# Kernel optimization log

Measured on AMD Instinct MI355X. Metric: run time of the kernel, lower is better.

The kernel has to match this reference:

```python
import jax, jax.numpy as jnp
import numpy as np
import math

B, T, M, C = 4, 2048, 16, 256   # batch, seq, m chunks, c_s chunk width
DIM = 1024                       # layer width; k = DIM // C = 4
D = 64                           # conditioning bottleneck
N_ITERS, TAU = 20, 1.0


def _diag_bias(rows, cols):
    b = np.full((rows, cols), -8.0, dtype=np.float32)
    for i in range(min(rows, cols)):
        b[i, i] = 0.0
    return jnp.asarray(b)


def setup_inputs() -> dict:
    key = jax.random.key(0)
    ks = jax.random.split(key, 10)
    state_dim = M * C
    k = DIM // C
    H_post = np.full((M, k), -8.0, dtype=np.float32)
    for i in range(M):
        H_post[i, i % k] = 0.0
    return {
        "s": jax.random.normal(ks[0], (B, T, M, C), jnp.float32),
        "gamma": 0.02 * jax.random.normal(ks[1], (state_dim,), jnp.float32),
        "compress": 0.02 * jax.random.normal(ks[2], (state_dim, D), jnp.float32),
        "alpha_pre": jnp.float32(0.01),
        "to_logits_pre": 0.02 * jax.random.normal(ks[3], (D, k * M), jnp.float32),
        "H_pre": _diag_bias(k, M),
        "alpha_align": jnp.float32(0.01),
        "to_logits_align": 0.02 * jax.random.normal(ks[4], (D, M * M), jnp.float32),
        "H_align": _diag_bias(M, M),
        "alpha_next": jnp.float32(0.01),
        "to_logits_next": 0.02 * jax.random.normal(ks[5], (D, M * M), jnp.float32),
        "H_next": _diag_bias(M, M),
        "alpha_post": jnp.float32(0.01),
        "to_logits_post": 0.02 * jax.random.normal(ks[6], (D, M * k), jnp.float32),
        "H_post": jnp.asarray(H_post),
        "W_layer": jax.random.normal(ks[7], (DIM, DIM), jnp.float32) / math.sqrt(DIM),
    }


def sinkhorn_log(logits, num_iters=N_ITERS, tau=TAU):
    """Log-domain Sinkhorn; output row-scaled so row sums = 1 * rows-normalized."""
    rows, cols = logits.shape[-2], logits.shape[-1]
    Z = logits / tau
    lr = -math.log(rows)
    lc = -math.log(cols)
    u0 = jnp.zeros(Z.shape[:-1], Z.dtype)
    v0 = jnp.zeros(Z.shape[:-2] + (cols,), Z.dtype)

    def body(_, uv):
        u, v = uv
        u = lr - jax.nn.logsumexp(Z + v[..., None, :], axis=-1)
        v = lc - jax.nn.logsumexp(Z + u[..., None], axis=-2)
        return (u, v)

    u, v = jax.lax.fori_loop(0, num_iters, body, (u0, v0))
    return jnp.exp(Z + u[..., None] + v[..., None, :]) * rows


def _route(code, alpha, to_logits, bias, state, rows, cols):
    """Fused: Sinkhorn(alpha*(code@to_logits)+bias) @ state."""
    raw = (code @ to_logits).reshape(code.shape[:-1] + (rows, cols))
    P = sinkhorn_log(alpha * raw + bias)
    return jnp.einsum('...ij,...jc->...ic', P, state)


def reference(s, gamma, compress, alpha_pre, to_logits_pre, H_pre,
              alpha_align, to_logits_align, H_align,
              alpha_next, to_logits_next, H_next,
              alpha_post, to_logits_post, H_post, W_layer):
    b, t, m, c = s.shape
    state_dim = m * c
    k = W_layer.shape[0] // c
    # RMSNorm over flattened state: F.normalize * sqrt(dim) * (gamma + 1)
    s_vec = s.reshape(b, t, state_dim)
    l2 = jnp.sqrt(jnp.sum(s_vec * s_vec, axis=-1, keepdims=True))
    s_norm = s_vec / jnp.maximum(l2, 1e-12) * jnp.sqrt(jnp.float32(state_dim)) * (gamma + 1.0)
    code = s_norm @ compress  # (b, t, d)
    # read: H_pre (k x m) routes state -> layer input
    layer_in = _route(code, alpha_pre, to_logits_pre, H_pre, s, k, m).reshape(b, t, k * c)
    layer_out = layer_in @ W_layer  # the wrapped layer_fn (dense linear)
    # write: align, absorb output via H_post, prepare next via H_next
    s_aligned = _route(code, alpha_align, to_logits_align, H_align, s, m, m)
    out_flat = layer_out.reshape(b, t, k, c)
    s_updated = s_aligned + _route(code, alpha_post, to_logits_post, H_post, out_flat, m, k)
    s_next = _route(code, alpha_next, to_logits_next, H_next, s_updated, m, m)
    return s_next
```

## Files before the change

kernel.cpp:

```cpp
#include <hip/hip_runtime.h>
#include <math.h>

#define NTOK 8192
#define SD   4096
#define ITERS 20

typedef __attribute__((ext_vector_type(8))) short short8;
typedef __attribute__((ext_vector_type(8))) unsigned short ushort8;
typedef __attribute__((ext_vector_type(4))) unsigned short us4;
typedef __attribute__((ext_vector_type(4))) float f32x4;

__device__ inline unsigned short f2bf(float x) {
    unsigned int u = __float_as_uint(x);
    unsigned int r = (u + 0x7FFFu + ((u >> 16) & 1u)) >> 16;
    return (unsigned short)r;
}
__device__ inline float bf2f(unsigned short u) {
    return __uint_as_float((unsigned int)u << 16);
}

__global__ __launch_bounds__(256) void k_preall(const float* __restrict__ W, unsigned short* __restrict__ WT,
                                                const float* __restrict__ compress, const float* __restrict__ gamma,
                                                unsigned short* __restrict__ cgT,
                                                const float* __restrict__ tl_pre, const float* __restrict__ tl_al,
                                                const float* __restrict__ tl_nx,  const float* __restrict__ tl_po,
                                                unsigned short* __restrict__ tlT)
{
    const int b = blockIdx.x;
    const int tid = threadIdx.x;
    if (b < 256) {
        __shared__ float tb[64][65];
        const int k0 = (b >> 4) * 64, n0 = (b & 15) * 64;
        #pragma unroll 4
        for (int q = 0; q < 16; ++q) {
            const int idx = q * 256 + tid;
            const int r = idx >> 6, c = idx & 63;
            tb[r][c] = W[(size_t)(k0 + r) * 1024 + n0 + c];
        }
        __syncthreads();
        #pragma unroll 4
        for (int q = 0; q < 16; ++q) {
            const int idx = q * 256 + tid;
            const int n = idx >> 6, k = idx & 63;
            WT[(size_t)(n0 + n) * 1024 + k0 + k] = f2bf(tb[k][n]);
        }
    } else if (b < 320) {
        __shared__ float tb2[64][65];
        __shared__ float gsh[64];
        const int k0 = (b - 256) * 64;
        #pragma unroll 4
        for (int q = 0; q < 16; ++q) {
            const int idx = q * 256 + tid;
            const int r = idx >> 6, dd = idx & 63;
            tb2[r][dd] = compress[(size_t)(k0 + r) * 64 + dd];
        }
        if (tid < 64) gsh[tid] = gamma[k0 + tid] + 1.0f;
        __syncthreads();
        #pragma unroll 4
        for (int q = 0; q < 16; ++q) {
            const int idx = q * 256 + tid;
            const int d = idx >> 6, r = idx & 63;
            cgT[(size_t)d * SD + k0 + r] = f2bf(tb2[r][d] * gsh[r]);
        }
    } else {
        const int idx = (b - 320) * 256 + tid;
        const int k = idx / 640, n = idx - k * 640;
        float v;
        if (n < 64)       v = tl_pre[k * 64 + n];
        else if (n < 320) v = tl_al[k * 256 + (n - 64)];
        else if (n < 576) v = tl_nx[k * 256 + (n - 320)];
        else              v = tl_po[k * 64 + (n - 576)];
        tlT[(size_t)n * 64 + k] = f2bf(v);
    }
}

#define LGS 660
__global__ __launch_bounds__(256) void k_front2(const float* __restrict__ s,
                                                const unsigned short* __restrict__ cgT,
                                                const unsigned short* __restrict__ tlT,
                                                const float* __restrict__ a_pre_p, const float* __restrict__ H_pre,
                                                const float* __restrict__ a_al_p,  const float* __restrict__ H_al,
                                                const float* __restrict__ a_nx_p,  const float* __restrict__ H_nx,
                                                const float* __restrict__ a_po_p,  const float* __restrict__ H_po,
                                                float* __restrict__ Ppre,
                                                float* __restrict__ Pna, float* __restrict__ Pnp)
{
    __shared__ __align__(16) char smem[61440];
    unsigned short* code_sh  = (unsigned short*)(smem);
    float*          red      = (float*)(smem + 2304);
    unsigned short* lg_sh    = (unsigned short*)(smem + 2304);
    float*          Pal_sh   = (float*)(smem + 23424);
    float*          Pnx_sh   = (float*)(smem + 40064);
    float*          Ppo_sh   = (float*)(smem + 56704);
    float*          ssq_part = (float*)(smem + 61056);
    float*          ssq_sh   = (float*)(smem + 61312);

    const int tid  = threadIdx.x;
    const int lane = tid & 63;
    const int wid  = tid >> 6;
    const int tok0 = blockIdx.x * 16;
    const int row  = lane & 15;
    const int kq   = lane >> 4;
    const int wk   = wid * 32;

    float ssq = 0.f;
    f32x4 acc[4];
    #pragma unroll
    for (int ni = 0; ni < 4; ++ni) acc[ni] = (f32x4){0.f, 0.f, 0.f, 0.f};

    const float*          srow  = s   + (size_t)(tok0 + row) * SD + wk + kq * 8;
    const unsigned short* cgrow = cgT + wk + kq * 8;

    #pragma unroll 2
    for (int ks = 0; ks < 32; ++ks) {
        const int kg = ks * 128;
        float4 v0 = *(const float4*)(srow + kg);
        float4 v1 = *(const float4*)(srow + kg + 4);
        ssq += v0.x*v0.x + v0.y*v0.y + v0.z*v0.z + v0.w*v0.w
             + v1.x*v1.x + v1.y*v1.y + v1.z*v1.z + v1.w*v1.w;
        short8 a;
        a[0]=(short)f2bf(v0.x); a[1]=(short)f2bf(v0.y); a[2]=(short)f2bf(v0.z); a[3]=(short)f2bf(v0.w);
        a[4]=(short)f2bf(v1.x); a[5]=(short)f2bf(v1.y); a[6]=(short)f2bf(v1.z); a[7]=(short)f2bf(v1.w);
        short8 b[4];
        #pragma unroll
        for (int ni = 0; ni < 4; ++ni)
            b[ni] = *(const short8*)(cgrow + (size_t)(ni * 16 + row) * SD + kg);
        #pragma unroll
        for (int ni = 0; ni < 4; ++ni)
            acc[ni] = __builtin_amdgcn_mfma_f32_16x16x32_bf16(a, b[ni], acc[ni], 0, 0, 0);
    }

    ssq += __shfl_xor(ssq, 16);
    ssq += __shfl_xor(ssq, 32);
    if (lane < 16) ssq_part[wid * 16 + row] = ssq;

    #pragma unroll
    for (int ni = 0; ni < 4; ++ni)
        #pragma unroll
        for (int r = 0; r < 4; ++r)
            red[wid * 1088 + ((lane >> 4) * 4 + r) * 68 + ni * 16 + (lane & 15)] = acc[ni][r];
    __syncthreads();
    if (tid < 16) {
        float t = ssq_part[tid] + ssq_part[16 + tid] + ssq_part[32 + tid] + ssq_part[48 + tid];
        ssq_sh[tid] = 64.0f / fmaxf(sqrtf(t), 1e-12f);
    }
    __syncthreads();
    #pragma unroll
    for (int q = 0; q < 4; ++q) {
        const int idx = q * 256 + tid;
        const int tok = idx >> 6, d = idx & 63;
        float v = red[0 * 1088 + tok * 68 + d] + red[1 * 1088 + tok * 68 + d]
                + red[2 * 1088 + tok * 68 + d] + red[3 * 1088 + tok * 68 + d];
        code_sh[tok * 72 + d] = f2bf(v * ssq_sh[tok]);
    }
    __syncthreads();

    {
        f32x4 acc2[10];
        #pragma unroll
        for (int ni = 0; ni < 10; ++ni) acc2[ni] = (f32x4){0.f, 0.f, 0.f, 0.f};
        const int nbase = wid * 160;
        #pragma unroll
        for (int ks = 0; ks < 2; ++ks) {
            const int ko = ks * 32 + (lane >> 4) * 8;
            short8 a = *(const short8*)(code_sh + (lane & 15) * 72 + ko);
            #pragma unroll
            for (int ni = 0; ni < 10; ++ni) {
                short8 b = *(const short8*)(tlT + (size_t)(nbase + ni * 16 + (lane & 15)) * 64 + ko);
                acc2[ni] = __builtin_amdgcn_mfma_f32_16x16x32_bf16(a, b, acc2[ni], 0, 0, 0);
            }
        }
        #pragma unroll
        for (int ni = 0; ni < 10; ++ni)
            #pragma unroll
            for (int r = 0; r < 4; ++r)
                lg_sh[((lane >> 4) * 4 + r) * LGS + nbase + ni * 16 + (lane & 15)] = f2bf(acc2[ni][r]);
    }
    __syncthreads();

    const int t_in = lane >> 2;
    const int sub  = lane & 3;
    const int tok  = tok0 + t_in;

    if (wid < 2) {
        const float alpha = (wid == 0) ? (*a_al_p) : (*a_nx_p);
        const float* Hp   = ((wid == 0) ? H_al : H_nx) + sub * 64;
        const unsigned short* lgp = lg_sh + t_in * LGS + (wid == 0 ? 64 : 320) + sub * 64;
        float Km[4][16];
        #pragma unroll
        for (int rr = 0; rr < 4; ++rr)
            #pragma unroll
            for (int h = 0; h < 2; ++h) {
                ushort8 rv = *(const ushort8*)(lgp + rr * 16 + h * 8);
                float4 h0 = *(const float4*)(Hp + rr * 16 + h * 8);
                float4 h1 = *(const float4*)(Hp + rr * 16 + h * 8 + 4);
                Km[rr][h*8+0] = expf(alpha * bf2f(rv[0]) + h0.x);
                Km[rr][h*8+1] = expf(alpha * bf2f(rv[1]) + h0.y);
                Km[rr][h*8+2] = expf(alpha * bf2f(rv[2]) + h0.z);
                Km[rr][h*8+3] = expf(alpha * bf2f(rv[3]) + h0.w);
                Km[rr][h*8+4] = expf(alpha * bf2f(rv[4]) + h1.x);
                Km[rr][h*8+5] = expf(alpha * bf2f(rv[5]) + h1.y);
                Km[rr][h*8+6] = expf(alpha * bf2f(rv[6]) + h1.z);
                Km[rr][h*8+7] = expf(alpha * bf2f(rv[7]) + h1.w);
            }
        float v[16], u[4];
        #pragma unroll
        for (int c = 0; c < 16; ++c) v[c] = 1.0f;
        for (int it = 0; it < ITERS; ++it) {
            #pragma unroll
            for (int rr = 0; rr < 4; ++rr) {
                float su = 0.f;
                #pragma unroll
                for (int c = 0; c < 16; ++c) su += Km[rr][c] * v[c];
                u[rr] = 0.0625f * __builtin_amdgcn_rcpf(su);
            }
            float pv[16];
            #pragma unroll
            for (int c = 0; c < 16; ++c)
                pv[c] = Km[0][c]*u[0] + Km[1][c]*u[1] + Km[2][c]*u[2] + Km[3][c]*u[3];
            #pragma unroll
            for (int c = 0; c < 16; ++c) pv[c] += __shfl_xor(pv[c], 1);
            #pragma unroll
            for (int c = 0; c < 16; ++c) pv[c] += __shfl_xor(pv[c], 2);
            #pragma unroll
            for (int c = 0; c < 16; ++c) v[c] = 0.0625f * __builtin_amdgcn_rcpf(pv[c]);
        }
        float* dst = ((wid == 0) ? Pal_sh : Pnx_sh) + t_in * 260;
        #pragma unroll
        for (int rr = 0; rr < 4; ++rr) {
            const float su16 = 16.0f * u[rr];
            #pragma unroll
            for (int c = 0; c < 16; ++c)
                dst[(sub * 4 + rr) * 16 + c] = Km[rr][c] * su16 * v[c];
        }
    } else if (wid == 2) {
        const float alpha = *a_pre_p;
        const unsigned short* lgp = lg_sh + t_in * LGS + sub * 16;
        const float* Hp  = H_pre + sub * 16;
        float Km[16];
        #pragma unroll
        for (int h = 0; h < 2; ++h) {
            ushort8 rv = *(const ushort8*)(lgp + h * 8);
            float4 h0 = *(const float4*)(Hp + h * 8);
            float4 h1 = *(const float4*)(Hp + h * 8 + 4);
            Km[h*8+0] = expf(alpha * bf2f(rv[0]) + h0.x);
            Km[h*8+1] = expf(alpha * bf2f(rv[1]) + h0.y);
            Km[h*8+2] = expf(alpha * bf2f(rv[2]) + h0.z);
            Km[h*8+3] = expf(alpha * bf2f(rv[3]) + h0.w);
            Km[h*8+4] = expf(alpha * bf2f(rv[4]) + h1.x);
            Km[h*8+5] = expf(alpha * bf2f(rv[5]) + h1.y);
            Km[h*8+6] = expf(alpha * bf2f(rv[6]) + h1.z);
            Km[h*8+7] = expf(alpha * bf2f(rv[7]) + h1.w);
        }
        float v[16], u;
        #pragma unroll
        for (int c = 0; c < 16; ++c) v[c] = 1.0f;
        for (int it = 0; it < ITERS; ++it) {
            float su = 0.f;
            #pragma unroll
            for (int c = 0; c < 16; ++c) su += Km[c] * v[c];
            u = 0.25f * __builtin_amdgcn_rcpf(su);
            float pv[16];
            #pragma unroll
            for (int c = 0; c < 16; ++c) pv[c] = Km[c] * u;
            #pragma unroll
            for (int c = 0; c < 16; ++c) pv[c] += __shfl_xor(pv[c], 1);
            #pragma unroll
            for (int c = 0; c < 16; ++c) pv[c] += __shfl_xor(pv[c], 2);
            #pragma unroll
            for (int c = 0; c < 16; ++c) v[c] = 0.0625f * __builtin_amdgcn_rcpf(pv[c]);
        }
        const float su4 = 4.0f * u;
        #pragma unroll
        for (int c = 0; c < 16; ++c)
            Ppre[(size_t)tok * 64 + sub * 16 + c] = Km[c] * su4 * v[c];
    } else {
        const float alpha = *a_po_p;
        const unsigned short* lgp = lg_sh + t_in * LGS + 576 + sub * 16;
        const float* Hp  = H_po + sub * 16;
        float Km[4][4];
        #pragma unroll
        for (int rr = 0; rr < 4; ++rr) {
            us4 rv = *(const us4*)(lgp + rr * 4);
            float4 hv = *(const float4*)(Hp + rr * 4);
            Km[rr][0] = expf(alpha * bf2f(rv[0]) + hv.x);
            Km[rr][1] = expf(alpha * bf2f(rv[1]) + hv.y);
            Km[rr][2] = expf(alpha * bf2f(rv[2]) + hv.z);
            Km[rr][3] = expf(alpha * bf2f(rv[3]) + hv.w);
        }
        float v[4], u[4];
        #pragma unroll
        for (int c = 0; c < 4; ++c) v[c] = 1.0f;
        for (int it = 0; it < ITERS; ++it) {
            #pragma unroll
            for (int rr = 0; rr < 4; ++rr) {
                float su = 0.f;
                #pragma unroll
                for (int c = 0; c < 4; ++c) su += Km[rr][c] * v[c];
                u[rr] = 0.0625f * __builtin_amdgcn_rcpf(su);
            }
            float pv[4];
            #pragma unroll
            for (int c = 0; c < 4; ++c)
                pv[c] = Km[0][c]*u[0] + Km[1][c]*u[1] + Km[2][c]*u[2] + Km[3][c]*u[3];
            #pragma unroll
            for (int c = 0; c < 4; ++c) pv[c] += __shfl_xor(pv[c], 1);
            #pragma unroll
            for (int c = 0; c < 4; ++c) pv[c] += __shfl_xor(pv[c], 2);
            #pragma unroll
            for (int c = 0; c < 4; ++c) v[c] = 0.25f * __builtin_amdgcn_rcpf(pv[c]);
        }
        #pragma unroll
        for (int rr = 0; rr < 4; ++rr) {
            const float su16 = 16.0f * u[rr];
            #pragma unroll
            for (int c = 0; c < 4; ++c)
                Ppo_sh[t_in * 68 + (sub * 4 + rr) * 4 + c] = Km[rr][c] * su16 * v[c];
        }
    }
    __syncthreads();

    const int ct = tid >> 4;
    const int cj = tid & 15;
    const float* pnx = Pnx_sh + ct * 260;
    const float* pal = Pal_sh + ct * 260;
    const float* ppo = Ppo_sh + ct * 68;
    #pragma unroll
    for (int m = 0; m < 16; ++m) {
        float a2 = 0.f;
        #pragma unroll
        for (int t2 = 0; t2 < 16; ++t2) a2 += pnx[m * 16 + t2] * pal[t2 * 16 + cj];
        Pna[(size_t)(tok0 + ct) * 256 + m * 16 + cj] = a2;
    }
    #pragma unroll
    for (int e = 0; e < 4; ++e) {
        const int idx = cj * 4 + e;
        const int m = idx >> 2, q = idx & 3;
        float a2 = 0.f;
        #pragma unroll
        for (int t2 = 0; t2 < 16; ++t2) a2 += pnx[m * 16 + t2] * ppo[t2 * 4 + q];
        Pnp[(size_t)(tok0 + ct) * 64 + idx] = a2;
    }
}

__global__ __launch_bounds__(256) void k_apply(const float* __restrict__ s,
                                               const float* __restrict__ Ppre,
                                               unsigned short* __restrict__ layer_in)
{
    __shared__ float s_sh[SD];
    __shared__ float P_sh[64];
    const int tid = threadIdx.x;
    const int tok = blockIdx.x;

    {
        const float4* sp4 = (const float4*)(s + (size_t)tok * SD);
        #pragma unroll
        for (int j = 0; j < 4; ++j)
            *(float4*)(s_sh + j * 1024 + tid * 4) = sp4[j * 256 + tid];
    }
    if (tid < 64) P_sh[tid] = Ppre[(size_t)tok * 64 + tid];
    __syncthreads();

    #pragma unroll
    for (int i = 0; i < 4; ++i) {
        float acc = 0.f;
        #pragma unroll
        for (int j = 0; j < 16; ++j) acc += P_sh[i * 16 + j] * s_sh[j * 256 + tid];
        layer_in[(size_t)tok * 1024 + i * 256 + tid] = f2bf(acc);
    }
}

__global__ __launch_bounds__(256) void k_gemm_bf16(const unsigned short* __restrict__ A,
                                                   const unsigned short* __restrict__ BT,
                                                   unsigned short* __restrict__ Cb)
{
    __shared__ unsigned short Abuf[128 * 48];
    __shared__ unsigned short Bbuf[128 * 48];
    const int tid  = threadIdx.x;
    const int lane = tid & 63;
    const int wid  = tid >> 6;
    const int wr   = wid >> 1, wc = wid & 1;
    const int m0 = blockIdx.y * 128, n0 = blockIdx.x * 128;

    f32x4 acc[4][4];
    #pragma unroll
    for (int mi = 0; mi < 4; ++mi)
        #pragma unroll
        for (int ni = 0; ni < 4; ++ni) acc[mi][ni] = (f32x4){0.f, 0.f, 0.f, 0.f};

    for (int k0 = 0; k0 < 1024; k0 += 32) {
        __syncthreads();
        #pragma unroll
        for (int h = 0; h < 2; ++h) {
            const int idx = h * 256 + tid;
            const int row = idx >> 2, kq = idx & 3;
            float4 av = *(const float4*)(A + (size_t)(m0 + row) * 1024 + k0 + kq * 8);
            *(float4*)(Abuf + row * 48 + kq * 8) = av;
            float4 bv = *(const float4*)(BT + (size_t)(n0 + row) * 1024 + k0 + kq * 8);
            *(float4*)(Bbuf + row * 48 + kq * 8) = bv;
        }
        __syncthreads();

        short8 a[4], b[4];
        #pragma unroll
        for (int mi = 0; mi < 4; ++mi)
            a[mi] = *(const short8*)(Abuf + (wr * 64 + mi * 16 + (lane & 15)) * 48 + (lane >> 4) * 8);
        #pragma unroll
        for (int ni = 0; ni < 4; ++ni)
            b[ni] = *(const short8*)(Bbuf + (wc * 64 + ni * 16 + (lane & 15)) * 48 + (lane >> 4) * 8);
        #pragma unroll
        for (int mi = 0; mi < 4; ++mi)
            #pragma unroll
            for (int ni = 0; ni < 4; ++ni)
                acc[mi][ni] = __builtin_amdgcn_mfma_f32_16x16x32_bf16(a[mi], b[ni], acc[mi][ni], 0, 0, 0);
    }

    #pragma unroll
    for (int mi = 0; mi < 4; ++mi)
        #pragma unroll
        for (int ni = 0; ni < 4; ++ni)
            #pragma unroll
            for (int r = 0; r < 4; ++r)
                Cb[(size_t)(m0 + wr * 64 + mi * 16 + (lane >> 4) * 4 + r) * 1024 +
                   n0 + wc * 64 + ni * 16 + (lane & 15)] = f2bf(acc[mi][ni][r]);
}

__global__ __launch_bounds__(256) void k_final(const float* __restrict__ s,
                                               const unsigned short* __restrict__ lo_bf,
                                               const float* __restrict__ Pna,
                                               const float* __restrict__ Pnp,
                                               float* __restrict__ out)
{
    __shared__ float s_sh[SD];
    __shared__ float lo_sh[1024];
    __shared__ float Pna_sh[256];
    __shared__ float Pnp_sh[64];
    const int tid = threadIdx.x;
    const int tok = blockIdx.x;

    {
        const float4* sp4 = (const float4*)(s + (size_t)tok * SD);
        #pragma unroll
        for (int j = 0; j < 4; ++j)
            *(float4*)(s_sh + j * 1024 + tid * 4) = sp4[j * 256 + tid];
    }
    {
        us4 lv = *(const us4*)(lo_bf + (size_t)tok * 1024 + tid * 4);
        float4 f;
        f.x = bf2f(lv[0]); f.y = bf2f(lv[1]); f.z = bf2f(lv[2]); f.w = bf2f(lv[3]);
        *(float4*)(lo_sh + tid * 4) = f;
    }
    Pna_sh[tid] = Pna[(size_t)tok * 256 + tid];
    if (tid < 64) Pnp_sh[tid] = Pnp[(size_t)tok * 64 + tid];
    __syncthreads();

    const int c = tid;
    #pragma unroll
    for (int m = 0; m < 16; ++m) {
        float acc = 0.f;
        #pragma unroll
        for (int j = 0; j < 16; ++j) acc += Pna_sh[m * 16 + j] * s_sh[j * 256 + c];
        #pragma unroll
        for (int q = 0; q < 4; ++q) acc += Pnp_sh[m * 4 + q] * lo_sh[q * 256 + c];
        out[(size_t)tok * SD + m * 256 + c] = acc;
    }
}

extern "C" void kernel_launch(void* const* d_in, const int* in_sizes, int n_in,
                              void* d_out, int out_size, void* d_ws, size_t ws_size,
                              hipStream_t stream)
{
    const float* s        = (const float*)d_in[0];
    const float* gamma    = (const float*)d_in[1];
    const float* compress = (const float*)d_in[2];
    const float* a_pre    = (const float*)d_in[3];
    const float* tl_pre   = (const float*)d_in[4];
    const float* H_pre    = (const float*)d_in[5];
    const float* a_al     = (const float*)d_in[6];
    const float* tl_al    = (const float*)d_in[7];
    const float* H_al     = (const float*)d_in[8];
    const float* a_nx     = (const float*)d_in[9];
    const float* tl_nx    = (const float*)d_in[10];
    const float* H_nx     = (const float*)d_in[11];
    const float* a_po     = (const float*)d_in[12];
    const float* tl_po    = (const float*)d_in[13];
    const float* H_po     = (const float*)d_in[14];
    const float* W        = (const float*)d_in[15];
    float* out = (float*)d_out;

    char* p = (char*)d_ws;
    unsigned short* lo_bf    = (unsigned short*)p; p += (size_t)8192 * 1024 * 2;
    float* Pna               = (float*)p;          p += (size_t)8192 * 256 * 4;
    float* Pnp               = (float*)p;          p += (size_t)8192 * 64 * 4;
    unsigned short* layer_in = (unsigned short*)p; p += (size_t)8192 * 1024 * 2;
    unsigned short* WT       = (unsigned short*)p; p += (size_t)1024 * 1024 * 2;
    unsigned short* cgT      = (unsigned short*)p; p += (size_t)64 * SD * 2;
    unsigned short* tlT      = (unsigned short*)p; p += (size_t)640 * 64 * 2 + 128;
    float* Ppre              = (float*)p;          p += (size_t)8192 * 64 * 4;

    k_preall<<<480, 256, 0, stream>>>(W, WT, compress, gamma, cgT,
                                      tl_pre, tl_al, tl_nx, tl_po, tlT);
    k_front2<<<512, 256, 0, stream>>>(s, cgT, tlT,
                                      a_pre, H_pre, a_al, H_al,
                                      a_nx, H_nx, a_po, H_po,
                                      Ppre, Pna, Pnp);
    k_apply<<<NTOK, 256, 0, stream>>>(s, Ppre, layer_in);
    k_gemm_bf16<<<dim3(8, 64), 256, 0, stream>>>(layer_in, WT, lo_bf);
    k_final<<<NTOK, 256, 0, stream>>>(s, lo_bf, Pna, Pnp, out);
}
```

Baseline: 195.7 us.

## Split front kernel into split-K code GEMM and separate Sinkhorn kernel

The fused front kernel is split in two. The first kernel computes the compress projection and sum of squares with a 4-way split over K on a 4x512 grid, writing fp32 partials. The second kernel sums those partials, normalizes, runs the logits MFMA and then the Sinkhorn iterations. The goal is more parallelism for the memory-bound read of s, since 512 blocks each streaming 4096 columns underfill the device. Shared memory is reduced, logits are staged into registers so the LDS can be reused, and expf is replaced with __expf. The cost is an extra launch and a round trip of partials through global memory.

Result: no change. 199.0 us (+1.7%).

```diff
diff --git a/kernel.cpp b/kernel.cpp
--- a/kernel.cpp
+++ b/kernel.cpp
@@ -74,45 +74,33 @@
     }
 }
 
-#define LGS 660
-__global__ __launch_bounds__(256) void k_front2(const float* __restrict__ s,
-                                                const unsigned short* __restrict__ cgT,
-                                                const unsigned short* __restrict__ tlT,
-                                                const float* __restrict__ a_pre_p, const float* __restrict__ H_pre,
-                                                const float* __restrict__ a_al_p,  const float* __restrict__ H_al,
-                                                const float* __restrict__ a_nx_p,  const float* __restrict__ H_nx,
-                                                const float* __restrict__ a_po_p,  const float* __restrict__ H_po,
-                                                float* __restrict__ Ppre,
-                                                float* __restrict__ Pna, float* __restrict__ Pnp)
-{
-    __shared__ __align__(16) char smem[61440];
-    unsigned short* code_sh  = (unsigned short*)(smem);
-    float*          red      = (float*)(smem + 2304);
-    unsigned short* lg_sh    = (unsigned short*)(smem + 2304);
-    float*          Pal_sh   = (float*)(smem + 23424);
-    float*          Pnx_sh   = (float*)(smem + 40064);
-    float*          Ppo_sh   = (float*)(smem + 56704);
-    float*          ssq_part = (float*)(smem + 61056);
-    float*          ssq_sh   = (float*)(smem + 61312);
-
+__global__ __launch_bounds__(256) void k_code5(const float* __restrict__ s,
+                                               const unsigned short* __restrict__ cgT,
+                                               float* __restrict__ code_part,
+                                               float* __restrict__ ssq_part)
+{
+    __shared__ float red[4 * 16 * 68];
+    __shared__ float ssq_lds[64];
     const int tid  = threadIdx.x;
     const int lane = tid & 63;
     const int wid  = tid >> 6;
-    const int tok0 = blockIdx.x * 16;
+    const int q    = blockIdx.x;
+    const int tok0 = blockIdx.y * 16;
     const int row  = lane & 15;
     const int kq   = lane >> 4;
     const int wk   = wid * 32;
+    const int kbase = q * 1024;
 
     float ssq = 0.f;
     f32x4 acc[4];
     #pragma unroll
     for (int ni = 0; ni < 4; ++ni) acc[ni] = (f32x4){0.f, 0.f, 0.f, 0.f};
 
-    const float*          srow  = s   + (size_t)(tok0 + row) * SD + wk + kq * 8;
-    const unsigned short* cgrow = cgT + wk + kq * 8;
-
-    #pragma unroll 2
-    for (int ks = 0; ks < 32; ++ks) {
+    const float*          srow  = s   + (size_t)(tok0 + row) * SD + kbase + wk + kq * 8;
+    const unsigned short* cgrow = cgT + kbase + wk + kq * 8;
+
+    #pragma unroll
+    for (int ks = 0; ks < 8; ++ks) {
         const int kg = ks * 128;
         float4 v0 = *(const float4*)(srow + kg);
         float4 v1 = *(const float4*)(srow + kg + 4);
@@ -132,7 +120,7 @@
 
     ssq += __shfl_xor(ssq, 16);
     ssq += __shfl_xor(ssq, 32);
-    if (lane < 16) ssq_part[wid * 16 + row] = ssq;
+    if (lane < 16) ssq_lds[wid * 16 + row] = ssq;
 
     #pragma unroll
     for (int ni = 0; ni < 4; ++ni)
@@ -140,18 +128,61 @@
         for (int r = 0; r < 4; ++r)
             red[wid * 1088 + ((lane >> 4) * 4 + r) * 68 + ni * 16 + (lane & 15)] = acc[ni][r];
     __syncthreads();
-    if (tid < 16) {
-        float t = ssq_part[tid] + ssq_part[16 + tid] + ssq_part[32 + tid] + ssq_part[48 + tid];
-        ssq_sh[tid] = 64.0f / fmaxf(sqrtf(t), 1e-12f);
-    }
-    __syncthreads();
-    #pragma unroll
-    for (int q = 0; q < 4; ++q) {
-        const int idx = q * 256 + tid;
+    if (tid < 16)
+        ssq_part[(size_t)q * NTOK + tok0 + tid] =
+            ssq_lds[tid] + ssq_lds[16 + tid] + ssq_lds[32 + tid] + ssq_lds[48 + tid];
+    #pragma unroll
+    for (int q2 = 0; q2 < 4; ++q2) {
+        const int idx = q2 * 256 + tid;
         const int tok = idx >> 6, d = idx & 63;
         float v = red[0 * 1088 + tok * 68 + d] + red[1 * 1088 + tok * 68 + d]
                 + red[2 * 1088 + tok * 68 + d] + red[3 * 1088 + tok * 68 + d];
-        code_sh[tok * 72 + d] = f2bf(v * ssq_sh[tok]);
+        code_part[((size_t)q * NTOK + tok0 + tok) * 64 + d] = v;
+    }
+}
+
+#define LGS 660
+__global__ __launch_bounds__(256) void k_sink3(const float* __restrict__ code_part,
+                                               const float* __restrict__ ssq_part,
+                                               const unsigned short* __restrict__ tlT,
+                                               const float* __restrict__ a_pre_p, const float* __restrict__ H_pre,
+                                               const float* __restrict__ a_al_p,  const float* __restrict__ H_al,
+                                               const float* __restrict__ a_nx_p,  const float* __restrict__ H_nx,
+                                               const float* __restrict__ a_po_p,  const float* __restrict__ H_po,
+                                               float* __restrict__ Ppre,
+                                               float* __restrict__ Pna, float* __restrict__ Pnp)
+{
+    __shared__ __align__(16) char smem[44480];
+    unsigned short* code_sh = (unsigned short*)(smem);
+    unsigned short* lg_sh   = (unsigned short*)(smem + 2304);
+    float*          Pnx_sh  = (float*)(smem + 2304);
+    float*          Pal_sh  = (float*)(smem + 23424);
+    float*          Ppo_sh  = (float*)(smem + 40064);
+    float*          ssq_sh  = (float*)(smem + 44416);
+
+    const int tid  = threadIdx.x;
+    const int lane = tid & 63;
+    const int wid  = tid >> 6;
+    const int tok0 = blockIdx.x * 16;
+
+    float cv[4];
+    #pragma unroll
+    for (int q2 = 0; q2 < 4; ++q2) {
+        const int idx = q2 * 256 + tid;
+        const size_t off = (size_t)(tok0 + (idx >> 6)) * 64 + (idx & 63);
+        cv[q2] = code_part[off] + code_part[(size_t)NTOK * 64 + off]
+               + code_part[(size_t)2 * NTOK * 64 + off] + code_part[(size_t)3 * NTOK * 64 + off];
+    }
+    if (tid < 16) {
+        float t = ssq_part[tok0 + tid] + ssq_part[NTOK + tok0 + tid]
+                + ssq_part[2 * NTOK + tok0 + tid] + ssq_part[3 * NTOK + tok0 + tid];
+        ssq_sh[tid] = 64.0f / fmaxf(sqrtf(t), 1e-12f);
+    }
+    __syncthreads();
+    #pragma unroll
+    for (int q2 = 0; q2 < 4; ++q2) {
+        const int idx = q2 * 256 + tid;
+        code_sh[(idx >> 6) * 72 + (idx & 63)] = f2bf(cv[q2] * ssq_sh[idx >> 6]);
     }
     __syncthreads();
 
@@ -181,28 +212,45 @@
     const int t_in = lane >> 2;
     const int sub  = lane & 3;
     const int tok  = tok0 + t_in;
+    float Km[4][16];
+
+    if (wid < 2) {
+        const unsigned short* lgp = lg_sh + t_in * LGS + (wid == 0 ? 64 : 320) + sub * 64;
+        #pragma unroll
+        for (int rr = 0; rr < 4; ++rr)
+            #pragma unroll
+            for (int h = 0; h < 2; ++h) {
+                ushort8 rv = *(const ushort8*)(lgp + rr * 16 + h * 8);
+                #pragma unroll
+                for (int e = 0; e < 8; ++e) Km[rr][h * 8 + e] = bf2f(rv[e]);
+            }
+    } else if (wid == 2) {
+        const unsigned short* lgp = lg_sh + t_in * LGS + sub * 16;
+        #pragma unroll
+        for (int h = 0; h < 2; ++h) {
+            ushort8 rv = *(const ushort8*)(lgp + h * 8);
+            #pragma unroll
+            for (int e = 0; e < 8; ++e) Km[0][h * 8 + e] = bf2f(rv[e]);
+        }
+    } else {
+        const unsigned short* lgp = lg_sh + t_in * LGS + 576 + sub * 16;
+        #pragma unroll
+        for (int rr = 0; rr < 4; ++rr) {
+            us4 rv = *(const us4*)(lgp + rr * 4);
+            #pragma unroll
+            for (int e = 0; e < 4; ++e) Km[rr][e] = bf2f(rv[e]);
+        }
+    }
+    __syncthreads();
 
     if (wid < 2) {
         const float alpha = (wid == 0) ? (*a_al_p) : (*a_nx_p);
         const float* Hp   = ((wid == 0) ? H_al : H_nx) + sub * 64;
-        const unsigned short* lgp = lg_sh + t_in * LGS + (wid == 0 ? 64 : 320) + sub * 64;
-        float Km[4][16];
         #pragma unroll
         for (int rr = 0; rr < 4; ++rr)
             #pragma unroll
-            for (int h = 0; h < 2; ++h) {
-                ushort8 rv = *(const ushort8*)(lgp + rr * 16 + h * 8);
-                float4 h0 = *(const float4*)(Hp + rr * 16 + h * 8);
-                float4 h1 = *(const float4*)(Hp + rr * 16 + h * 8 + 4);
-                Km[rr][h*8+0] = expf(alpha * bf2f(rv[0]) + h0.x);
-                Km[rr][h*8+1] = expf(alpha * bf2f(rv[1]) + h0.y);
-                Km[rr][h*8+2] = expf(alpha * bf2f(rv[2]) + h0.z);
-                Km[rr][h*8+3] = expf(alpha * bf2f(rv[3]) + h0.w);
-                Km[rr][h*8+4] = expf(alpha * bf2f(rv[4]) + h1.x);
-                Km[rr][h*8+5] = expf(alpha * bf2f(rv[5]) + h1.y);
-                Km[rr][h*8+6] = expf(alpha * bf2f(rv[6]) + h1.z);
-                Km[rr][h*8+7] = expf(alpha * bf2f(rv[7]) + h1.w);
-            }
+            for (int c = 0; c < 16; ++c)
+                Km[rr][c] = __expf(alpha * Km[rr][c] + Hp[rr * 16 + c]);
         float v[16], u[4];
         #pragma unroll
         for (int c = 0; c < 16; ++c) v[c] = 1.0f;
@@ -235,34 +283,20 @@
         }
     } else if (wid == 2) {
         const float alpha = *a_pre_p;
-        const unsigned short* lgp = lg_sh + t_in * LGS + sub * 16;
         const float* Hp  = H_pre + sub * 16;
-        float Km[16];
-        #pragma unroll
-        for (int h = 0; h < 2; ++h) {
-            ushort8 rv = *(const ushort8*)(lgp + h * 8);
-            float4 h0 = *(const float4*)(Hp + h * 8);
-            float4 h1 = *(const float4*)(Hp + h * 8 + 4);
-            Km[h*8+0] = expf(alpha * bf2f(rv[0]) + h0.x);
-            Km[h*8+1] = expf(alpha * bf2f(rv[1]) + h0.y);
-            Km[h*8+2] = expf(alpha * bf2f(rv[2]) + h0.z);
-            Km[h*8+3] = expf(alpha * bf2f(rv[3]) + h0.w);
-            Km[h*8+4] = expf(alpha * bf2f(rv[4]) + h1.x);
-            Km[h*8+5] = expf(alpha * bf2f(rv[5]) + h1.y);
-            Km[h*8+6] = expf(alpha * bf2f(rv[6]) + h1.z);
-            Km[h*8+7] = expf(alpha * bf2f(rv[7]) + h1.w);
-        }
+        #pragma unroll
+        for (int c = 0; c < 16; ++c) Km[0][c] = __expf(alpha * Km[0][c] + Hp[c]);
         float v[16], u;
         #pragma unroll
         for (int c = 0; c < 16; ++c) v[c] = 1.0f;
         for (int it = 0; it < ITERS; ++it) {
             float su = 0.f;
             #pragma unroll
-            for (int c = 0; c < 16; ++c) su += Km[c] * v[c];
+            for (int c = 0; c < 16; ++c) su += Km[0][c] * v[c];
             u = 0.25f * __builtin_amdgcn_rcpf(su);
             float pv[16];
             #pragma unroll
-            for (int c = 0; c < 16; ++c) pv[c] = Km[c] * u;
+            for (int c = 0; c < 16; ++c) pv[c] = Km[0][c] * u;
             #pragma unroll
             for (int c = 0; c < 16; ++c) pv[c] += __shfl_xor(pv[c], 1);
             #pragma unroll
@@ -273,21 +307,15 @@
         const float su4 = 4.0f * u;
         #pragma unroll
         for (int c = 0; c < 16; ++c)
-            Ppre[(size_t)tok * 64 + sub * 16 + c] = Km[c] * su4 * v[c];
+            Ppre[(size_t)tok * 64 + sub * 16 + c] = Km[0][c] * su4 * v[c];
     } else {
         const float alpha = *a_po_p;
-        const unsigned short* lgp = lg_sh + t_in * LGS + 576 + sub * 16;
         const float* Hp  = H_po + sub * 16;
-        float Km[4][4];
-        #pragma unroll
-        for (int rr = 0; rr < 4; ++rr) {
-            us4 rv = *(const us4*)(lgp + rr * 4);
-            float4 hv = *(const float4*)(Hp + rr * 4);
-            Km[rr][0] = expf(alpha * bf2f(rv[0]) + hv.x);
-            Km[rr][1] = expf(alpha * bf2f(rv[1]) + hv.y);
-            Km[rr][2] = expf(alpha * bf2f(rv[2]) + hv.z);
-            Km[rr][3] = expf(alpha * bf2f(rv[3]) + hv.w);
-        }
+        #pragma unroll
+        for (int rr = 0; rr < 4; ++rr)
+            #pragma unroll
+            for (int c = 0; c < 4; ++c)
+                Km[rr][c] = __expf(alpha * Km[rr][c] + Hp[rr * 4 + c]);
         float v[4], u[4];
         #pragma unroll
         for (int c = 0; c < 4; ++c) v[c] = 1.0f;
@@ -497,13 +525,16 @@
     unsigned short* cgT      = (unsigned short*)p; p += (size_t)64 * SD * 2;
     unsigned short* tlT      = (unsigned short*)p; p += (size_t)640 * 64 * 2 + 128;
     float* Ppre              = (float*)p;          p += (size_t)8192 * 64 * 4;
+    float* code_part         = (float*)p;          p += (size_t)4 * NTOK * 64 * 4;
+    float* ssq_part          = (float*)p;          p += (size_t)4 * NTOK * 4;
 
     k_preall<<<480, 256, 0, stream>>>(W, WT, compress, gamma, cgT,
                                       tl_pre, tl_al, tl_nx, tl_po, tlT);
-    k_front2<<<512, 256, 0, stream>>>(s, cgT, tlT,
-                                      a_pre, H_pre, a_al, H_al,
-                                      a_nx, H_nx, a_po, H_po,
-                                      Ppre, Pna, Pnp);
+    k_code5<<<dim3(4, 512), 256, 0, stream>>>(s, cgT, code_part, ssq_part);
+    k_sink3<<<512, 256, 0, stream>>>(code_part, ssq_part, tlT,
+                                     a_pre, H_pre, a_al, H_al,
+                                     a_nx, H_nx, a_po, H_po,
+                                     Ppre, Pna, Pnp);
     k_apply<<<NTOK, 256, 0, stream>>>(s, Ppre, layer_in);
     k_gemm_bf16<<<dim3(8, 64), 256, 0, stream>>>(layer_in, WT, lo_bf);
     k_final<<<NTOK, 256, 0, stream>>>(s, lo_bf, Pna, Pnp, out);
```
